# Kernel tuning notes

Measured on AMD Instinct MI355X. Metric: run time of the kernel, lower is better.

The kernel has to match this reference:

```python
import jax, jax.numpy as jnp
import numpy as np

N_QUBITS = 4
N_LAYERS = 2
DIM = 2 ** N_QUBITS
B, S, E = 4, 512, 512


def _apply_ry_batched(state, theta, wire):
    # per-element RY data-encoding; state: [N, 2,2,2,2], theta: [N]
    ax = wire + 1
    half = theta * 0.5
    bshape = (-1,) + (1,) * (N_QUBITS - 1)
    c = jnp.cos(half).reshape(bshape)
    s = jnp.sin(half).reshape(bshape)
    s0 = jnp.take(state, 0, axis=ax)
    s1 = jnp.take(state, 1, axis=ax)
    return jnp.stack([c * s0 - s * s1, s * s0 + c * s1], axis=ax)


def _rot_gate(w3):
    # combined RZ(c) @ RY(b) @ RX(a), 2x2 complex (applied RX first)
    a, b, c = w3[0] * 0.5, w3[1] * 0.5, w3[2] * 0.5
    ca, sa = jnp.cos(a), jnp.sin(a)
    cb, sb = jnp.cos(b), jnp.sin(b)
    RX = jnp.array([[ca + 0j, -1j * sa], [-1j * sa, ca + 0j]])
    RY = jnp.array([[cb + 0j, -sb + 0j], [sb + 0j, cb + 0j]])
    ez = jnp.exp(-1j * c)
    RZ = jnp.array([[ez, 0j], [0j, jnp.conj(ez)]])
    return (RZ @ RY @ RX).astype(jnp.complex64)


def _apply_gate(state, gate, wire):
    s = jnp.tensordot(state, gate, axes=([wire + 1], [1]))
    return jnp.moveaxis(s, -1, wire + 1)


def _apply_cnot(state, ctrl, tgt):
    s = jnp.moveaxis(state, (ctrl + 1, tgt + 1), (1, 2))
    s = jnp.stack([s[:, 0], s[:, 1, ::-1]], axis=1)
    return jnp.moveaxis(s, (1, 2), (ctrl + 1, tgt + 1))


def _quantum_scores(angles, weights):
    # angles: [N, N_QUBITS] real; returns [N] = sum_i <Z_i>
    n = angles.shape[0]
    state = jnp.zeros((n, DIM), jnp.complex64).at[:, 0].set(1.0)
    state = state.reshape((n,) + (2,) * N_QUBITS)
    for w in range(N_QUBITS):
        state = _apply_ry_batched(state, angles[:, w], w)
    wmat = weights.reshape(N_LAYERS, N_QUBITS, 3)
    for layer in range(N_LAYERS):
        for w in range(N_QUBITS):
            state = _apply_gate(state, _rot_gate(wmat[layer, w]), w)
        for w in range(N_QUBITS - 1):
            state = _apply_cnot(state, w, w + 1)
        if N_QUBITS > 2:
            state = _apply_cnot(state, N_QUBITS - 1, 0)
    probs = (state.real ** 2 + state.imag ** 2).reshape(n, DIM)
    idx = np.arange(DIM)
    bits = (idx[:, None] >> np.arange(N_QUBITS)) & 1  # [DIM, n_qubits]
    zvec = jnp.asarray((1 - 2 * bits).sum(axis=1), jnp.float32)  # sum_i (-1)^bit_i
    return probs @ zvec


def setup_inputs() -> dict:
    key = jax.random.key(0)
    ks = jax.random.split(key, 8)
    x = jax.random.normal(ks[0], (B, S, E), jnp.float32)
    def lin(kk, fi, fo):
        return jax.random.normal(kk, (fi, fo), jnp.float32) / np.sqrt(fi)
    Wq = lin(ks[1], E, N_QUBITS)
    Wk = lin(ks[2], E, N_QUBITS)
    Wv = lin(ks[3], E, N_QUBITS)
    Wout = lin(ks[4], N_QUBITS, E)
    bq = 0.1 * jax.random.normal(ks[5], (N_QUBITS,), jnp.float32)
    bk = 0.1 * jax.random.normal(ks[6], (N_QUBITS,), jnp.float32)
    bv = jnp.zeros((N_QUBITS,), jnp.float32)
    bout = jnp.zeros((E,), jnp.float32)
    quantum_weights = 0.1 * jax.random.normal(ks[7], (N_LAYERS * N_QUBITS * 3,), jnp.float32)
    return {"x": x, "Wq": Wq, "bq": bq, "Wk": Wk, "bk": bk, "Wv": Wv, "bv": bv,
            "quantum_weights": quantum_weights, "Wout": Wout, "bout": bout}


def reference(x, Wq, bq, Wk, bk, Wv, bv, quantum_weights, Wout, bout):
    b, s, e = x.shape
    q = jnp.tanh(x @ Wq + bq)          # [B,S,nq]
    k = jnp.tanh(x @ Wk + bk)          # [B,S,nq]
    v = x @ Wv + bv                    # [B,S,nq]
    # pairwise circuit inputs: tanh(q_i + k_j) for all (b,i,j)
    angles = jnp.tanh(q[:, :, None, :] + k[:, None, :, :]).reshape(-1, N_QUBITS)
    scores = _quantum_scores(angles, quantum_weights).reshape(b, s, s)
    attn = jax.nn.softmax(scores / np.sqrt(N_QUBITS), axis=-1)
    attended = jnp.einsum('bij,bjd->bid', attn, v)
    out = attended @ Wout + bout       # [B,S,E]
    return out, attn
```

## Files before the change

kernel.cpp:

```cpp
#include <hip/hip_runtime.h>
#include <math.h>

#define NQ 4
#define DIM 16
#define BB 4
#define SS 512
#define EE 512
#define ROWS (BB * SS)

__global__ __launch_bounds__(256) void k_prep(
    const float* __restrict__ x,
    const float* __restrict__ Wq, const float* __restrict__ bq,
    const float* __restrict__ Wk, const float* __restrict__ bk,
    const float* __restrict__ Wv, const float* __restrict__ bv,
    const float* __restrict__ qw,
    float* __restrict__ tq, float* __restrict__ tk, float* __restrict__ v,
    float* __restrict__ T_out) {
    if (blockIdx.x == 0) {
        __shared__ float sG[8][8];
        __shared__ float Ur[DIM][DIM];
        __shared__ float Ui[DIM][DIM];
        __shared__ float sMr[256];
        int t = threadIdx.x;
        if (t < 8) {
            float a = qw[t * 3 + 0] * 0.5f;
            float b = qw[t * 3 + 1] * 0.5f;
            float c = qw[t * 3 + 2] * 0.5f;
            float sa = __sinf(a), ca = __cosf(a);
            float sb = __sinf(b), cb = __cosf(b);
            float sc = __sinf(c), cc = __cosf(c);
            float m00r = cb * ca, m00i = sb * sa;
            float m01r = -sb * ca, m01i = -cb * sa;
            float m10r = sb * ca, m10i = -cb * sa;
            float m11r = cb * ca, m11i = -sb * sa;
            sG[t][0] = cc * m00r + sc * m00i;
            sG[t][1] = cc * m00i - sc * m00r;
            sG[t][2] = cc * m01r + sc * m01i;
            sG[t][3] = cc * m01i - sc * m01r;
            sG[t][4] = cc * m10r - sc * m10i;
            sG[t][5] = cc * m10i + sc * m10r;
            sG[t][6] = cc * m11r - sc * m11i;
            sG[t][7] = cc * m11i + sc * m11r;
        }
        __syncthreads();
        if (t < DIM) {
            float vr[DIM], vi[DIM];
#pragma unroll
            for (int i = 0; i < DIM; ++i) { vr[i] = (i == t) ? 1.f : 0.f; vi[i] = 0.f; }
#pragma unroll
            for (int gi = 0; gi < 8; ++gi) {
                int w = gi & 3;
                float g00r = sG[gi][0], g00i = sG[gi][1];
                float g01r = sG[gi][2], g01i = sG[gi][3];
                float g10r = sG[gi][4], g10i = sG[gi][5];
                float g11r = sG[gi][6], g11i = sG[gi][7];
                int mask = 1 << (3 - w);
#pragma unroll
                for (int idx = 0; idx < DIM; ++idx) {
                    if (idx & mask) continue;
                    int i1 = idx | mask;
                    float r0 = vr[idx], i0 = vi[idx], r1 = vr[i1], i1v = vi[i1];
                    vr[idx] = g00r * r0 - g00i * i0 + g01r * r1 - g01i * i1v;
                    vi[idx] = g00r * i0 + g00i * r0 + g01r * i1v + g01i * r1;
                    vr[i1]  = g10r * r0 - g10i * i0 + g11r * r1 - g11i * i1v;
                    vi[i1]  = g10r * i0 + g10i * r0 + g11r * i1v + g11i * r1;
                }
                if (w == 3) {
                    const int cwire[4] = {0, 1, 2, 3};
                    const int twire[4] = {1, 2, 3, 0};
#pragma unroll
                    for (int e = 0; e < 4; ++e) {
                        int cmask = 1 << (3 - cwire[e]);
                        int tmask = 1 << (3 - twire[e]);
                        float nr[DIM], ni[DIM];
#pragma unroll
                        for (int idx = 0; idx < DIM; ++idx) {
                            int src = (idx & cmask) ? (idx ^ tmask) : idx;
                            nr[idx] = vr[src]; ni[idx] = vi[src];
                        }
#pragma unroll
                        for (int idx = 0; idx < DIM; ++idx) { vr[idx] = nr[idx]; vi[idx] = ni[idx]; }
                    }
                }
            }
#pragma unroll
            for (int i = 0; i < DIM; ++i) { Ur[i][t] = vr[i]; Ui[i][t] = vi[i]; }
        }
        __syncthreads();
        {
            int k = t >> 4, l = t & 15;
            float acc = 0.f;
#pragma unroll
            for (int idx = 0; idx < DIM; ++idx) {
                float z = 4.f - 2.f * (float)__popc(idx);
                acc += z * (Ur[idx][k] * Ur[idx][l] + Ui[idx][k] * Ui[idx][l]);
            }
            sMr[t] = acc;
        }
        __syncthreads();
        if (t < 81) {
            int e3 = t % 3, e2 = (t / 3) % 3, e1 = (t / 9) % 3, e0 = t / 27;
            int xm = ((e0 == 2) << 3) | ((e1 == 2) << 2) | ((e2 == 2) << 1) | (int)(e3 == 2);
            int sm = ((e0 == 1) << 3) | ((e1 == 1) << 2) | ((e2 == 1) << 1) | (int)(e3 == 1);
            float acc = 0.f;
#pragma unroll
            for (int K = 0; K < DIM; ++K) {
                float s = (__popc(K & sm) & 1) ? -1.f : 1.f;
                acc += s * sMr[K * 16 + (K ^ xm)];
            }
            T_out[((e0 * 3 + e1) * 3 + e2) * 4 + e3] = acc * (1.f / 32.f);
        }
        if (t < 27) T_out[t * 4 + 3] = 0.f;
    } else {
        int row = (blockIdx.x - 1) * 4 + (threadIdx.x >> 6);
        int lane = threadIdx.x & 63;
        const float* xr = x + (size_t)row * EE;
        float aq[4] = {0, 0, 0, 0}, ak[4] = {0, 0, 0, 0}, av[4] = {0, 0, 0, 0};
        for (int e = lane; e < EE; e += 64) {
            float xv = xr[e];
            float4 wq = *(const float4*)(Wq + e * 4);
            float4 wk = *(const float4*)(Wk + e * 4);
            float4 wv = *(const float4*)(Wv + e * 4);
            aq[0] += xv * wq.x; aq[1] += xv * wq.y; aq[2] += xv * wq.z; aq[3] += xv * wq.w;
            ak[0] += xv * wk.x; ak[1] += xv * wk.y; ak[2] += xv * wk.z; ak[3] += xv * wk.w;
            av[0] += xv * wv.x; av[1] += xv * wv.y; av[2] += xv * wv.z; av[3] += xv * wv.w;
        }
#pragma unroll
        for (int off = 32; off > 0; off >>= 1) {
#pragma unroll
            for (int c = 0; c < 4; ++c) {
                aq[c] += __shfl_down(aq[c], off, 64);
                ak[c] += __shfl_down(ak[c], off, 64);
                av[c] += __shfl_down(av[c], off, 64);
            }
        }
        if (lane == 0) {
#pragma unroll
            for (int c = 0; c < 4; ++c) {
                tq[row * 4 + c] = tanhf(tanhf(aq[c] + bq[c]));
                tk[row * 4 + c] = tanhf(tanhf(ak[c] + bk[c]));
                v[row * 4 + c] = av[c] + bv[c];
            }
        }
    }
}

__global__ __launch_bounds__(256) void k_attn(
    const float* __restrict__ tq, const float* __restrict__ tk,
    const float* __restrict__ v, const float* __restrict__ Tg,
    const float* __restrict__ Wout, const float* __restrict__ bout,
    float* __restrict__ attn_out, float* __restrict__ out) {
    int row = blockIdx.x;
    int b = row >> 9;
    int tid = threadIdx.x;
    int wid = tid >> 6, lane = tid & 63;
    int j0 = tid, j1 = tid + 256;

    __shared__ float4 sT[27];
    __shared__ float rmax[4], rsum[4], rv[4][4];

    if (tid < 27) sT[tid] = ((const float4*)Tg)[tid];
    __syncthreads();

    const float4 q4 = *(const float4*)(tq + row * 4);
    const float4 ka = *(const float4*)(tk + (size_t)(b * SS + j0) * 4);
    const float4 kb = *(const float4*)(tk + (size_t)(b * SS + j1) * 4);

    float t0a = (q4.x + ka.x) / fmaf(q4.x, ka.x, 1.f);
    float t1a = (q4.y + ka.y) / fmaf(q4.y, ka.y, 1.f);
    float t2a = (q4.z + ka.z) / fmaf(q4.z, ka.z, 1.f);
    float t3a = (q4.w + ka.w) / fmaf(q4.w, ka.w, 1.f);
    float t0b = (q4.x + kb.x) / fmaf(q4.x, kb.x, 1.f);
    float t1b = (q4.y + kb.y) / fmaf(q4.y, kb.y, 1.f);
    float t2b = (q4.z + kb.z) / fmaf(q4.z, kb.z, 1.f);
    float t3b = (q4.w + kb.w) / fmaf(q4.w, kb.w, 1.f);

    float c0a = __cosf(t0a), s0a = __sinf(t0a);
    float c1a = __cosf(t1a), s1a = __sinf(t1a);
    float c2a = __cosf(t2a), s2a = __sinf(t2a);
    float c3a = __cosf(t3a), s3a = __sinf(t3a);
    float c0b = __cosf(t0b), s0b = __sinf(t0b);
    float c1b = __cosf(t1b), s1b = __sinf(t1b);
    float c2b = __cosf(t2b), s2b = __sinf(t2b);
    float c3b = __cosf(t3b), s3b = __sinf(t3b);

    float u0a[3] = {1.f, c0a, s0a}, u1a[3] = {1.f, c1a, s1a}, u2a[3] = {1.f, c2a, s2a};
    float u0b[3] = {1.f, c0b, s0b}, u1b[3] = {1.f, c1b, s1b}, u2b[3] = {1.f, c2b, s2b};

    float sc_a = 0.f, sc_b = 0.f;
#pragma unroll
    for (int e0 = 0; e0 < 3; ++e0) {
        float a1a = 0.f, a1b = 0.f;
#pragma unroll
        for (int e1 = 0; e1 < 3; ++e1) {
            float a2a = 0.f, a2b = 0.f;
#pragma unroll
            for (int e2 = 0; e2 < 3; ++e2) {
                float4 Tv = sT[(e0 * 3 + e1) * 3 + e2];
                float ia = fmaf(s3a, Tv.z, fmaf(c3a, Tv.y, Tv.x));
                float ib = fmaf(s3b, Tv.z, fmaf(c3b, Tv.y, Tv.x));
                a2a = fmaf(u2a[e2], ia, a2a);
                a2b = fmaf(u2b[e2], ib, a2b);
            }
            a1a = fmaf(u1a[e1], a2a, a1a);
            a1b = fmaf(u1b[e1], a2b, a1b);
        }
        sc_a = fmaf(u0a[e0], a1a, sc_a);
        sc_b = fmaf(u0b[e0], a1b, sc_b);
    }

    float m = fmaxf(sc_a, sc_b);
#pragma unroll
    for (int off = 32; off > 0; off >>= 1) m = fmaxf(m, __shfl_xor(m, off, 64));
    if (lane == 0) rmax[wid] = m;
    __syncthreads();
    float bm = fmaxf(fmaxf(rmax[0], rmax[1]), fmaxf(rmax[2], rmax[3]));

    float ex_a = __expf(sc_a - bm);
    float ex_b = __expf(sc_b - bm);
    float sum = ex_a + ex_b;
#pragma unroll
    for (int off = 32; off > 0; off >>= 1) sum += __shfl_xor(sum, off, 64);
    if (lane == 0) rsum[wid] = sum;
    __syncthreads();
    float bs = rsum[0] + rsum[1] + rsum[2] + rsum[3];
    float inv = 1.f / bs;
    float wa = ex_a * inv, wb = ex_b * inv;

    attn_out[(size_t)row * SS + j0] = wa;
    attn_out[(size_t)row * SS + j1] = wb;

    const float4 va = *(const float4*)(v + (size_t)(b * SS + j0) * 4);
    const float4 vb = *(const float4*)(v + (size_t)(b * SS + j1) * 4);
    float p[4];
    p[0] = wa * va.x + wb * vb.x;
    p[1] = wa * va.y + wb * vb.y;
    p[2] = wa * va.z + wb * vb.z;
    p[3] = wa * va.w + wb * vb.w;
#pragma unroll
    for (int w = 0; w < 4; ++w) {
#pragma unroll
        for (int off = 32; off > 0; off >>= 1) p[w] += __shfl_xor(p[w], off, 64);
        if (lane == 0) rv[wid][w] = p[w];
    }
    __syncthreads();

    float a0 = rv[0][0] + rv[1][0] + rv[2][0] + rv[3][0];
    float a1 = rv[0][1] + rv[1][1] + rv[2][1] + rv[3][1];
    float a2 = rv[0][2] + rv[1][2] + rv[2][2] + rv[3][2];
    float a3 = rv[0][3] + rv[1][3] + rv[2][3] + rv[3][3];
    int e = tid * 2;
    float2 w0 = *(const float2*)(Wout + 0 * EE + e);
    float2 w1 = *(const float2*)(Wout + 1 * EE + e);
    float2 w2 = *(const float2*)(Wout + 2 * EE + e);
    float2 w3 = *(const float2*)(Wout + 3 * EE + e);
    float2 bb = *(const float2*)(bout + e);
    float2 o;
    o.x = fmaf(a0, w0.x, fmaf(a1, w1.x, fmaf(a2, w2.x, fmaf(a3, w3.x, bb.x))));
    o.y = fmaf(a0, w0.y, fmaf(a1, w1.y, fmaf(a2, w2.y, fmaf(a3, w3.y, bb.y))));
    *(float2*)(out + (size_t)row * EE + e) = o;
}

extern "C" void kernel_launch(void* const* d_in, const int* in_sizes, int n_in,
                              void* d_out, int out_size, void* d_ws, size_t ws_size,
                              hipStream_t stream) {
    const float* x    = (const float*)d_in[0];
    const float* Wq   = (const float*)d_in[1];
    const float* bq   = (const float*)d_in[2];
    const float* Wk   = (const float*)d_in[3];
    const float* bk   = (const float*)d_in[4];
    const float* Wv   = (const float*)d_in[5];
    const float* bv   = (const float*)d_in[6];
    const float* qw   = (const float*)d_in[7];
    const float* Wout = (const float*)d_in[8];
    const float* bout = (const float*)d_in[9];

    float* out  = (float*)d_out;
    float* attn = out + (size_t)ROWS * EE;

    float* ws  = (float*)d_ws;
    float* T   = ws;
    float* tq  = ws + 128;
    float* tk  = tq + ROWS * 4;
    float* v   = tk + ROWS * 4;

    k_prep<<<1 + ROWS / 4, 256, 0, stream>>>(x, Wq, bq, Wk, bk, Wv, bv, qw, tq, tk, v, T);
    k_attn<<<ROWS, 256, 0, stream>>>(tq, tk, v, T, Wout, bout, attn, out);
}
```

Before: 89.94 us.

## Drop softmax max pass and fuse sum with value reductions; vectorize x loads

The attention kernel no longer computes a row max before exponentiating. It relies on the quantum scores being bounded (a sum of four Z expectations scaled by the constant folded into T, so exp cannot overflow), which removes one block-wide reduction and one barrier. The softmax denominator and the four weighted value sums are reduced together in one shuffle pass and normalised afterwards. Separately, the projection kernel reads x as float4 and uses explicit FMAs, which changes the weight access pattern so that each lane reads four consecutive weight rows.

```diff
diff --git a/kernel.cpp b/kernel.cpp
--- a/kernel.cpp
+++ b/kernel.cpp
@@ -114,16 +114,26 @@
     } else {
         int row = (blockIdx.x - 1) * 4 + (threadIdx.x >> 6);
         int lane = threadIdx.x & 63;
-        const float* xr = x + (size_t)row * EE;
+        const float4* xr4 = (const float4*)(x + (size_t)row * EE);
         float aq[4] = {0, 0, 0, 0}, ak[4] = {0, 0, 0, 0}, av[4] = {0, 0, 0, 0};
-        for (int e = lane; e < EE; e += 64) {
-            float xv = xr[e];
-            float4 wq = *(const float4*)(Wq + e * 4);
-            float4 wk = *(const float4*)(Wk + e * 4);
-            float4 wv = *(const float4*)(Wv + e * 4);
-            aq[0] += xv * wq.x; aq[1] += xv * wq.y; aq[2] += xv * wq.z; aq[3] += xv * wq.w;
-            ak[0] += xv * wk.x; ak[1] += xv * wk.y; ak[2] += xv * wk.z; ak[3] += xv * wk.w;
-            av[0] += xv * wv.x; av[1] += xv * wv.y; av[2] += xv * wv.z; av[3] += xv * wv.w;
+#pragma unroll
+        for (int h = 0; h < 2; ++h) {
+            int e4 = lane + h * 64;
+            float4 xv = xr4[e4];
+            float xc[4] = {xv.x, xv.y, xv.z, xv.w};
+#pragma unroll
+            for (int c = 0; c < 4; ++c) {
+                int e = e4 * 4 + c;
+                float4 wq = *(const float4*)(Wq + e * 4);
+                float4 wk = *(const float4*)(Wk + e * 4);
+                float4 wv = *(const float4*)(Wv + e * 4);
+                aq[0] = fmaf(xc[c], wq.x, aq[0]); aq[1] = fmaf(xc[c], wq.y, aq[1]);
+                aq[2] = fmaf(xc[c], wq.z, aq[2]); aq[3] = fmaf(xc[c], wq.w, aq[3]);
+                ak[0] = fmaf(xc[c], wk.x, ak[0]); ak[1] = fmaf(xc[c], wk.y, ak[1]);
+                ak[2] = fmaf(xc[c], wk.z, ak[2]); ak[3] = fmaf(xc[c], wk.w, ak[3]);
+                av[0] = fmaf(xc[c], wv.x, av[0]); av[1] = fmaf(xc[c], wv.y, av[1]);
+                av[2] = fmaf(xc[c], wv.z, av[2]); av[3] = fmaf(xc[c], wv.w, av[3]);
+            }
         }
 #pragma unroll
         for (int off = 32; off > 0; off >>= 1) {
@@ -157,7 +167,7 @@
     int j0 = tid, j1 = tid + 256;
 
     __shared__ float4 sT[27];
-    __shared__ float rmax[4], rsum[4], rv[4][4];
+    __shared__ float red[4][5];
 
     if (tid < 27) sT[tid] = ((const float4*)Tg)[tid];
     __syncthreads();
@@ -209,46 +219,39 @@
         sc_b = fmaf(u0b[e0], a1b, sc_b);
     }
 
-    float m = fmaxf(sc_a, sc_b);
-#pragma unroll
-    for (int off = 32; off > 0; off >>= 1) m = fmaxf(m, __shfl_xor(m, off, 64));
-    if (lane == 0) rmax[wid] = m;
-    __syncthreads();
-    float bm = fmaxf(fmaxf(rmax[0], rmax[1]), fmaxf(rmax[2], rmax[3]));
-
-    float ex_a = __expf(sc_a - bm);
-    float ex_b = __expf(sc_b - bm);
-    float sum = ex_a + ex_b;
-#pragma unroll
-    for (int off = 32; off > 0; off >>= 1) sum += __shfl_xor(sum, off, 64);
-    if (lane == 0) rsum[wid] = sum;
-    __syncthreads();
-    float bs = rsum[0] + rsum[1] + rsum[2] + rsum[3];
-    float inv = 1.f / bs;
-    float wa = ex_a * inv, wb = ex_b * inv;
-
-    attn_out[(size_t)row * SS + j0] = wa;
-    attn_out[(size_t)row * SS + j1] = wb;
+    float ex_a = __expf(sc_a);
+    float ex_b = __expf(sc_b);
 
     const float4 va = *(const float4*)(v + (size_t)(b * SS + j0) * 4);
     const float4 vb = *(const float4*)(v + (size_t)(b * SS + j1) * 4);
-    float p[4];
-    p[0] = wa * va.x + wb * vb.x;
-    p[1] = wa * va.y + wb * vb.y;
-    p[2] = wa * va.z + wb * vb.z;
-    p[3] = wa * va.w + wb * vb.w;
-#pragma unroll
-    for (int w = 0; w < 4; ++w) {
-#pragma unroll
-        for (int off = 32; off > 0; off >>= 1) p[w] += __shfl_xor(p[w], off, 64);
-        if (lane == 0) rv[wid][w] = p[w];
+    float vals[5];
+    vals[0] = ex_a + ex_b;
+    vals[1] = fmaf(ex_a, va.x, ex_b * vb.x);
+    vals[2] = fmaf(ex_a, va.y, ex_b * vb.y);
+    vals[3] = fmaf(ex_a, va.z, ex_b * vb.z);
+    vals[4] = fmaf(ex_a, va.w, ex_b * vb.w);
+#pragma unroll
+    for (int off = 32; off > 0; off >>= 1) {
+#pragma unroll
+        for (int c = 0; c < 5; ++c) vals[c] += __shfl_xor(vals[c], off, 64);
+    }
+    if (lane == 0) {
+#pragma unroll
+        for (int c = 0; c < 5; ++c) red[wid][c] = vals[c];
     }
     __syncthreads();
 
-    float a0 = rv[0][0] + rv[1][0] + rv[2][0] + rv[3][0];
-    float a1 = rv[0][1] + rv[1][1] + rv[2][1] + rv[3][1];
-    float a2 = rv[0][2] + rv[1][2] + rv[2][2] + rv[3][2];
-    float a3 = rv[0][3] + rv[1][3] + rv[2][3] + rv[3][3];
+    float tot = red[0][0] + red[1][0] + red[2][0] + red[3][0];
+    float inv = 1.f / tot;
+
+    attn_out[(size_t)row * SS + j0] = ex_a * inv;
+    attn_out[(size_t)row * SS + j1] = ex_b * inv;
+
+    float a0 = (red[0][1] + red[1][1] + red[2][1] + red[3][1]) * inv;
+    float a1 = (red[0][2] + red[1][2] + red[2][2] + red[3][2]) * inv;
+    float a2 = (red[0][3] + red[1][3] + red[2][3] + red[3][3]) * inv;
+    float a3 = (red[0][4] + red[1][4] + red[2][4] + red[3][4]) * inv;
+
     int e = tid * 2;
     float2 w0 = *(const float2*)(Wout + 0 * EE + e);
     float2 w1 = *(const float2*)(Wout + 1 * EE + e);
```

After: 87.85 us. -2.3%, faster.
